# Kernel tuning notes

Hardware: AMD Instinct MI355X
Metric: run time of the kernel (lower is better)

Reference implementation:

```python
import jax, jax.numpy as jnp
import numpy as np
from jax import lax


def conv2d(x, w, padding):
    # x: [B,C,H,W], w: [O,I,kh,kw]; torch Conv2d == cross-correlation, same as lax default
    return lax.conv_general_dilated(x, w, (1, 1), padding,
                                    dimension_numbers=('NCHW', 'OIHW', 'NCHW'))


def setup_inputs() -> dict:
    key = jax.random.key(0)
    ks = jax.random.split(key, 16)
    B, C1, C2, H1, W1, H2, W2, ratio = 8, 256, 512, 64, 64, 32, 32, 8
    Cr = C1 // ratio  # 32
    s = 0.05
    return {
        'x1': jax.random.normal(ks[0], (B, C1, H1, W1), jnp.float32),
        'x2': jax.random.normal(ks[1], (B, C2, H2, W2), jnp.float32),
        'wq': jax.random.normal(ks[2], (Cr, C1, 3, 3), jnp.float32) * s,
        'wk': jax.random.normal(ks[3], (Cr, C2, 3, 3), jnp.float32) * s,
        'wv': jax.random.normal(ks[4], (C1, C2, 3, 3), jnp.float32) * s,
        'wc': jax.random.normal(ks[5], (1, C1, 1, 1), jnp.float32) * s,
        'wch': jax.random.normal(ks[6], (C1, C1, 3, 3), jnp.float32) * s,
        'wt1': jax.random.normal(ks[7], (Cr, C1, 1, 1), jnp.float32) * s,
        'bt1': jax.random.normal(ks[8], (Cr,), jnp.float32) * s,
        'ln_g': jnp.ones((Cr, 1, 1), jnp.float32),
        'ln_b': jnp.zeros((Cr, 1, 1), jnp.float32),
        'wt2': jax.random.normal(ks[9], (C1, Cr, 1, 1), jnp.float32) * s,
        'bt2': jax.random.normal(ks[10], (C1,), jnp.float32) * s,
    }


def reference(x1, x2, wq, wk, wv, wc, wch, wt1, bt1, ln_g, ln_b, wt2, bt2):
    B, C1, H1, W1 = x1.shape
    N1 = H1 * W1
    N2 = x2.shape[2] * x2.shape[3]
    eps = 1e-5

    # spatial cross-attention branch
    q = conv2d(x1, wq, 'SAME').reshape(B, -1, N1)          # [B,Cr,N1]
    k = conv2d(x2, wk, 'SAME').reshape(B, -1, N2)          # [B,Cr,N2]
    v = conv2d(x2, wv, 'SAME').reshape(B, C1, N2)          # [B,C1,N2]
    content = jnp.einsum('bcn,bcm->bnm', k, q)             # [B,N2,N1] (key^T @ query)
    content = jax.nn.softmax(content, axis=1)              # softmax over N2 (dim=1)
    att_con = jnp.einsum('bcn,bnm->bcm', v, content).reshape(B, C1, H1, W1) + x1

    # channel attention branch
    cf = conv2d(x1, wc, 'VALID').reshape(B, 1, N1)         # 1x1 conv -> [B,1,N1]
    cf = jax.nn.softmax(cf.transpose(0, 2, 1), axis=1)     # [B,N1,1], softmax over N1
    chf = conv2d(x1, wch, 'SAME').reshape(B, C1, N1)       # [B,C1,N1]
    pool = jnp.einsum('bcn,bno->bco', chf, cf).reshape(B, C1, 1, 1)

    t = conv2d(pool, wt1, 'VALID') + bt1.reshape(1, -1, 1, 1)  # [B,Cr,1,1]
    mu = jnp.mean(t, axis=(1, 2, 3), keepdims=True)
    var = jnp.mean((t - mu) ** 2, axis=(1, 2, 3), keepdims=True)
    t = (t - mu) * lax.rsqrt(var + eps) * ln_g[None] + ln_b[None]
    t = jax.nn.relu(t)
    channel_weight = conv2d(t, wt2, 'VALID') + bt2.reshape(1, -1, 1, 1)  # [B,C1,1,1]

    return att_con + x1 * channel_weight
```

## Files before the change

kernel.cpp:

```cpp
#include <hip/hip_runtime.h>
#include <stdint.h>

#define LL long long

typedef short short8 __attribute__((ext_vector_type(8)));
typedef float f32x4 __attribute__((ext_vector_type(4)));
typedef unsigned int uint2v __attribute__((ext_vector_type(2)));

__device__ __forceinline__ unsigned short f2bf(float f) {
  unsigned u = __float_as_uint(f);
  unsigned r = (u + 0x7fffu + ((u >> 16) & 1u)) >> 16;
  return (unsigned short)r;
}
__device__ __forceinline__ float bf2f(unsigned short h) {
  return __uint_as_float(((unsigned)h) << 16);
}

#define MFMA16(A, B, C) __builtin_amdgcn_mfma_f32_16x16x32_bf16(A, B, C, 0, 0, 0)

__global__ __launch_bounds__(256) void wtrans2(
    const float* __restrict__ src, unsigned short* __restrict__ dh,
    unsigned short* __restrict__ dl, int OC, int IC)
{
  const int i = blockIdx.x * 256 + threadIdx.x;
  if (i >= OC * IC * 9) return;
  const int off = i % 9;
  const int rest = i / 9;
  const int ic = rest % IC;
  const int oc = rest / IC;
  const float v = src[i];
  const unsigned short h = f2bf(v);
  const LL di = (((LL)off * (IC >> 5) + (ic >> 5)) * OC + oc) * 32 + (ic & 31);
  dh[di] = h;
  if (dl) dl[di] = f2bf(v - bf2f(h));
}

__global__ __launch_bounds__(256) void transp(
    const float* __restrict__ src, unsigned short* __restrict__ dh,
    unsigned short* __restrict__ dl, int C, int N)
{
  __shared__ unsigned short sh[64 * 66];
  __shared__ unsigned short sl[64 * 66];
  const int t = threadIdx.x;
  const int b = blockIdx.z;
  const int n0 = blockIdx.x * 64, c0 = blockIdx.y * 64;
  {
    const int nl = t & 63, cl0 = t >> 6;
#pragma unroll
    for (int i = 0; i < 16; ++i) {
      const int cl = cl0 + 4 * i;
      const float v = src[((LL)b * C + c0 + cl) * N + n0 + nl];
      const unsigned short h = f2bf(v);
      sh[nl * 66 + cl] = h;
      sl[nl * 66 + cl] = f2bf(v - bf2f(h));
    }
  }
  __syncthreads();
  {
    const int cl = t & 63, nr0 = t >> 6;
    const int chunk = (c0 + cl) >> 5;
    const int cin = cl & 31;
#pragma unroll
    for (int j = 0; j < 16; ++j) {
      const int nr = nr0 + 4 * j;
      const LL di = (((LL)b * (C >> 5) + chunk) * N + n0 + nr) * 32 + cin;
      dh[di] = sh[nr * 66 + cl];
      if (dl) dl[di] = sl[nr * 66 + cl];
    }
  }
}

template<int NW>
__global__ __launch_bounds__(NW * 64) void conv_qk_s(
    const unsigned short* __restrict__ xh, const unsigned short* __restrict__ xl,
    const unsigned short* __restrict__ wh, const unsigned short* __restrict__ wl,
    unsigned short* __restrict__ dh, unsigned short* __restrict__ dl,
    int logW, int H)
{
  __shared__ float sred[NW][16][64];
  const int t = threadIdx.x, w = t >> 6, lane = t & 63;
  const int lo4 = lane & 15, hi4 = lane >> 4;
  const int b = blockIdx.z;
  const int W = 1 << logW;
  const int N = H * W;
  const int px0 = blockIdx.x * 32;
  const int row = px0 >> logW;
  const int x0 = px0 & (W - 1);
  const int ch = w;
  const short8 zero8 = {0, 0, 0, 0, 0, 0, 0, 0};

  f32x4 acc[2][2];
#pragma unroll
  for (int p = 0; p < 2; ++p)
#pragma unroll
    for (int ot = 0; ot < 2; ++ot) acc[p][ot] = (f32x4){0.f, 0.f, 0.f, 0.f};

  const LL xbase = ((LL)(b * NW + ch)) * N * 32 + hi4 * 8;
#pragma unroll
  for (int ky = 0; ky < 3; ++ky) {
    const int gy = row + ky - 1;
    const bool oky = (unsigned)gy < (unsigned)H;
    const int gyc = min(max(gy, 0), H - 1);
#pragma unroll
    for (int kx = 0; kx < 3; ++kx) {
      short8 Bh[2], Bl[2];
#pragma unroll
      for (int p = 0; p < 2; ++p) {
        const int gx = x0 + p * 16 + lo4 + kx - 1;
        const bool ok = oky && ((unsigned)gx < (unsigned)W);
        const int gxc = min(max(gx, 0), W - 1);
        const LL xoff = xbase + (LL)(gyc * W + gxc) * 32;
        const short8 bh = *(const short8*)(xh + xoff);
        const short8 bl = *(const short8*)(xl + xoff);
        Bh[p] = ok ? bh : zero8;
        Bl[p] = ok ? bl : zero8;
      }
      const int off = ky * 3 + kx;
      short8 Ah[2], Al[2];
#pragma unroll
      for (int ot = 0; ot < 2; ++ot) {
        const LL wi = ((LL)(off * NW + ch) * 32 + ot * 16 + lo4) * 32 + hi4 * 8;
        Ah[ot] = *(const short8*)(wh + wi);
        Al[ot] = *(const short8*)(wl + wi);
      }
#pragma unroll
      for (int p = 0; p < 2; ++p)
#pragma unroll
        for (int ot = 0; ot < 2; ++ot) {
          acc[p][ot] = MFMA16(Ah[ot], Bh[p], acc[p][ot]);
          acc[p][ot] = MFMA16(Ah[ot], Bl[p], acc[p][ot]);
          acc[p][ot] = MFMA16(Al[ot], Bh[p], acc[p][ot]);
        }
    }
  }
#pragma unroll
  for (int p = 0; p < 2; ++p)
#pragma unroll
    for (int ot = 0; ot < 2; ++ot)
#pragma unroll
      for (int r = 0; r < 4; ++r)
        sred[w][p * 8 + ot * 4 + r][lane] = acc[p][ot][r];
  __syncthreads();
  constexpr int SPW = 16 / NW;
#pragma unroll
  for (int si = 0; si < SPW; ++si) {
    const int slot = w * SPW + si;
    float v = sred[0][slot][lane];
#pragma unroll
    for (int j = 1; j < NW; ++j) v += sred[j][slot][lane];
    const int p = slot >> 3, ot = (slot >> 2) & 1, r = slot & 3;
    const LL di = ((LL)b * N + px0 + p * 16 + lo4) * 32 + ot * 16 + hi4 * 4 + r;
    const unsigned short h = f2bf(v);
    dh[di] = h;
    dl[di] = f2bf(v - bf2f(h));
  }
}

__global__ __launch_bounds__(512) void conv_v_w(
    const unsigned short* __restrict__ xh, const unsigned short* __restrict__ wt,
    unsigned short* __restrict__ out)
{
  __shared__ float sred[4][32][64];
  const int t = threadIdx.x, w = t >> 6, lane = t & 63;
  const int lo4 = lane & 15, hi4 = lane >> 4;
  const int b = blockIdx.z;
  const int h = w & 1, ocg = (w >> 1) & 1, kp = w >> 2;
  const int r0 = blockIdx.x * 4;
  const int ocb = blockIdx.y * 64 + ocg * 32;
  const short8 zero8 = {0, 0, 0, 0, 0, 0, 0, 0};

  f32x4 acc[4][2];
#pragma unroll
  for (int rr = 0; rr < 4; ++rr)
#pragma unroll
    for (int ot = 0; ot < 2; ++ot) acc[rr][ot] = (f32x4){0.f, 0.f, 0.f, 0.f};

  for (int ch = kp * 8; ch < kp * 8 + 8; ++ch) {
    short8 A[3][3][2];
#pragma unroll
    for (int ky = 0; ky < 3; ++ky)
#pragma unroll
      for (int kx = 0; kx < 3; ++kx)
#pragma unroll
        for (int ot = 0; ot < 2; ++ot) {
          const int off = ky * 3 + kx;
          A[ky][kx][ot] = *(const short8*)(
              wt + ((LL)(off * 16 + ch) * 256 + ocb + ot * 16 + lo4) * 32 + hi4 * 8);
        }
    const LL xchb = ((LL)(b * 16 + ch)) * 1024 * 32 + hi4 * 8;
#pragma unroll
    for (int g = 0; g < 6; ++g) {
      const int gy = r0 - 1 + g;
      const bool oky = (unsigned)gy < 32u;
      const int gyc = min(max(gy, 0), 31);
      short8 Bg[3];
#pragma unroll
      for (int kx = 0; kx < 3; ++kx) {
        const int gx = h * 16 + lo4 + kx - 1;
        const bool ok = oky && ((unsigned)gx < 32u);
        const int gxc = min(max(gx, 0), 31);
        const short8 bv = *(const short8*)(xh + xchb + (LL)(gyc * 32 + gxc) * 32);
        Bg[kx] = ok ? bv : zero8;
      }
#pragma unroll
      for (int rr = 0; rr < 4; ++rr) {
        if (rr > g || rr + 2 < g) continue;
        const int ky = g - rr;
#pragma unroll
        for (int kx = 0; kx < 3; ++kx)
#pragma unroll
          for (int ot = 0; ot < 2; ++ot)
            acc[rr][ot] = MFMA16(A[ky][kx][ot], Bg[kx], acc[rr][ot]);
      }
    }
  }
  const int slotbase = h * 2 + ocg;
  if (kp == 1) {
#pragma unroll
    for (int rr = 0; rr < 4; ++rr)
#pragma unroll
      for (int ot = 0; ot < 2; ++ot)
#pragma unroll
        for (int r = 0; r < 4; ++r)
          sred[slotbase][rr * 8 + ot * 4 + r][lane] = acc[rr][ot][r];
  }
  __syncthreads();
  if (kp == 0) {
#pragma unroll
    for (int rr = 0; rr < 4; ++rr)
#pragma unroll
      for (int ot = 0; ot < 2; ++ot)
#pragma unroll
        for (int r = 0; r < 4; ++r) {
          const float v = acc[rr][ot][r] + sred[slotbase][rr * 8 + ot * 4 + r][lane];
          const int row = r0 + rr;
          const int oc = ocb + ot * 16 + hi4 * 4 + r;
          out[(((LL)b * 32 + row) * 256 + oc) * 32 + h * 16 + lo4] = f2bf(v);
        }
  }
}

__global__ __launch_bounds__(256) void cf_dot(
    const float* __restrict__ x1, const float* __restrict__ wc, float* __restrict__ cf)
{
  const int b = blockIdx.y;
  const int n = blockIdx.x * 256 + threadIdx.x;
  const float* xp = x1 + (LL)b * 256 * 4096 + n;
  float a = 0.f;
#pragma unroll 4
  for (int c = 0; c < 256; ++c)
    a = fmaf(xp[(LL)c * 4096], wc[c], a);
  cf[b * 4096 + n] = a;
}

__global__ __launch_bounds__(1024) void cf_softmax(
    const float* __restrict__ cf, float* __restrict__ cfs)
{
  const int b = blockIdx.x, t = threadIdx.x;
  __shared__ float r1[16];
  __shared__ float r2[16];
  float v[4];
#pragma unroll
  for (int j = 0; j < 4; ++j) v[j] = cf[b * 4096 + t + 1024 * j];
  float mx = fmaxf(fmaxf(v[0], v[1]), fmaxf(v[2], v[3]));
#pragma unroll
  for (int k = 1; k <= 32; k <<= 1) mx = fmaxf(mx, __shfl_xor(mx, k));
  const int wv = t >> 6;
  if ((t & 63) == 0) r1[wv] = mx;
  __syncthreads();
  float m2 = r1[0];
#pragma unroll
  for (int i = 1; i < 16; ++i) m2 = fmaxf(m2, r1[i]);
  float e[4]; float s = 0.f;
#pragma unroll
  for (int j = 0; j < 4; ++j) { e[j] = __expf(v[j] - m2); s += e[j]; }
#pragma unroll
  for (int k = 1; k <= 32; k <<= 1) s += __shfl_xor(s, k);
  if ((t & 63) == 0) r2[wv] = s;
  __syncthreads();
  float s2 = 0.f;
#pragma unroll
  for (int i = 0; i < 16; ++i) s2 += r2[i];
  const float inv = 1.f / s2;
#pragma unroll
  for (int j = 0; j < 4; ++j) cfs[b * 4096 + t + 1024 * j] = e[j] * inv;
}

__global__ __launch_bounds__(512) void ykern2(
    const float* __restrict__ x1, const float* __restrict__ cfs,
    float* __restrict__ ykp)
{
  __shared__ __align__(16) float cl2[64][4];
  __shared__ float sredY[256][9];
  const int t = threadIdx.x;
  const int c = t & 255, h = t >> 8;
  const int bx = blockIdx.x, b = blockIdx.y;
  const int base = bx * 2;
  if (t < 256) {
    const int r = t >> 6, cc = t & 63;
    const int grow = base - 1 + r;
    cl2[cc][r] = ((unsigned)grow < 64u) ? cfs[b * 4096 + grow * 64 + cc] : 0.f;
  }
  __syncthreads();
  const int row = base + h;
  float xr[66];
  xr[0] = 0.f; xr[65] = 0.f;
  {
    const float4* xp = (const float4*)(x1 + ((LL)(b * 256 + c)) * 4096 + row * 64);
#pragma unroll
    for (int j = 0; j < 16; ++j) {
      const float4 v = xp[j];
      xr[1 + 4 * j] = v.x; xr[2 + 4 * j] = v.y;
      xr[3 + 4 * j] = v.z; xr[4 + 4 * j] = v.w;
    }
  }
  float a[9];
#pragma unroll
  for (int k = 0; k < 9; ++k) a[k] = 0.f;
  const bool h1 = (h == 1);
#pragma unroll
  for (int c0 = 0; c0 < 64; ++c0) {
    const float4 f4 = *(const float4*)&cl2[c0][0];
    const float f_dy0 = h1 ? f4.w : f4.z;
    const float f_dy1 = h1 ? f4.z : f4.y;
    const float f_dy2 = h1 ? f4.y : f4.x;
#pragma unroll
    for (int dx = 0; dx < 3; ++dx) {
      const float xv = xr[c0 + dx];
      a[0 * 3 + dx] = fmaf(xv, f_dy0, a[0 * 3 + dx]);
      a[1 * 3 + dx] = fmaf(xv, f_dy1, a[1 * 3 + dx]);
      a[2 * 3 + dx] = fmaf(xv, f_dy2, a[2 * 3 + dx]);
    }
  }
  if (h1) {
#pragma unroll
    for (int k = 0; k < 9; ++k) sredY[c][k] = a[k];
  }
  __syncthreads();
  if (!h1) {
    float* op = ykp + ((LL)(b * 32 + bx)) * 2304 + c * 9;
#pragma unroll
    for (int k = 0; k < 9; ++k) op[k] = a[k] + sredY[c][k];
  }
}

__global__ __launch_bounds__(256) void red_t(
    const float* __restrict__ src, float* __restrict__ dst)
{
  const int b = blockIdx.y;
  const int i = blockIdx.x * 256 + threadIdx.x;
  if (i >= 576) return;
  const f32x4* sp = (const f32x4*)(src + (LL)b * 32 * 2304);
  f32x4 a = sp[i];
  for (int p = 1; p < 32; ++p) a += sp[p * 576 + i];
  ((f32x4*)(dst + (LL)b * 2304))[i] = a;
}

__global__ __launch_bounds__(256) void pool_k(
    const float* __restrict__ T, const float* __restrict__ wch,
    float* __restrict__ pool)
{
  __shared__ __align__(16) float Tl[2304];
  const int b = blockIdx.y, ocg = blockIdx.x;
  const int t = threadIdx.x, w = t >> 6, lane = t & 63;
  for (int i = t; i < 2304; i += 256) Tl[i] = T[(LL)b * 2304 + i];
  __syncthreads();
  const float4* tp = (const float4*)Tl;
#pragma unroll
  for (int oi = 0; oi < 2; ++oi) {
    const int oc = ocg * 8 + w * 2 + oi;
    const float4* wp = (const float4*)(wch + (LL)oc * 2304);
    float a = 0.f;
#pragma unroll
    for (int j = 0; j < 9; ++j) {
      const int idx = lane + 64 * j;
      float4 w4 = wp[idx], t4 = tp[idx];
      a = fmaf(w4.x, t4.x, a); a = fmaf(w4.y, t4.y, a);
      a = fmaf(w4.z, t4.z, a); a = fmaf(w4.w, t4.w, a);
    }
#pragma unroll
    for (int k = 1; k <= 32; k <<= 1) a += __shfl_xor(a, k);
    if (lane == 0) pool[b * 256 + oc] = a;
  }
}

__global__ __launch_bounds__(256) void chw_tail(
    const float* __restrict__ pool_g,
    const float* __restrict__ wt1, const float* __restrict__ bt1,
    const float* __restrict__ lng, const float* __restrict__ lnb,
    const float* __restrict__ wt2, const float* __restrict__ bt2,
    float* __restrict__ cwp1)
{
  const int b = blockIdx.x, t = threadIdx.x;
  __shared__ float pool[256];
  __shared__ float tt[32];
  pool[t] = pool_g[b * 256 + t];
  __syncthreads();
  if (t < 64) {
    float tv = 0.f;
    if (t < 32) {
      const float* wp = wt1 + (LL)t * 256;
      for (int c = 0; c < 256; ++c) tv = fmaf(wp[c], pool[c], tv);
      tv += bt1[t];
    }
    float s = tv;
#pragma unroll
    for (int k = 1; k <= 16; k <<= 1) s += __shfl_xor(s, k);
    float mu = s * (1.f / 32.f);
    float d = tv - mu;
    float vs = d * d;
#pragma unroll
    for (int k = 1; k <= 16; k <<= 1) vs += __shfl_xor(vs, k);
    float var = vs * (1.f / 32.f);
    if (t < 32) {
      float nrm = d / sqrtf(var + 1e-5f);
      float y = nrm * lng[t] + lnb[t];
      tt[t] = fmaxf(y, 0.f);
    }
  }
  __syncthreads();
  {
    float s2 = bt2[t];
    const float* wp = wt2 + (LL)t * 32;
#pragma unroll
    for (int i = 0; i < 32; ++i) s2 = fmaf(wp[i], tt[i], s2);
    cwp1[b * 256 + t] = 1.f + s2;
  }
}

__global__ __launch_bounds__(256) void attn_stats(
    const unsigned short* __restrict__ qh_g, const unsigned short* __restrict__ ql_g,
    const unsigned short* __restrict__ kh_g, const unsigned short* __restrict__ kl_g,
    float* __restrict__ mxs, float* __restrict__ invl)
{
  const int t = threadIdx.x, w = t >> 6, lane = t & 63;
  const int lo4 = lane & 15, hi4 = lane >> 4;
  const int b = blockIdx.y, mc = blockIdx.x * 64;
  const float L2E = 1.4426950408889634f;

  short8 qh[4], ql[4];
#pragma unroll
  for (int mt = 0; mt < 4; ++mt) {
    const LL qa = ((LL)(b * 4096 + mc + mt * 16 + lo4)) * 32 + hi4 * 8;
    qh[mt] = *(const short8*)(qh_g + qa);
    ql[mt] = *(const short8*)(ql_g + qa);
  }

  float M[4], L[4];
#pragma unroll
  for (int mt = 0; mt < 4; ++mt) { M[mt] = -1e30f; L[mt] = 0.f; }

  for (int ns = 0; ns < 16; ++ns) {
    const int n = w * 256 + ns * 16 + lo4;
    const LL ka = ((LL)(b * 1024 + n)) * 32 + hi4 * 8;
    const short8 kh = *(const short8*)(kh_g + ka);
    const short8 kl = *(const short8*)(kl_g + ka);
#pragma unroll
    for (int mt = 0; mt < 4; ++mt) {
      f32x4 s = {0.f, 0.f, 0.f, 0.f};
      s = MFMA16(kl, qh[mt], s);
      s = MFMA16(kh, ql[mt], s);
      s = MFMA16(kh, qh[mt], s);
      float lm = fmaxf(fmaxf(s[0], s[1]), fmaxf(s[2], s[3]));
      float nM = fmaxf(M[mt], lm);
      float sc = exp2f((M[mt] - nM) * L2E);
      L[mt] = L[mt] * sc + exp2f((s[0] - nM) * L2E) + exp2f((s[1] - nM) * L2E)
                         + exp2f((s[2] - nM) * L2E) + exp2f((s[3] - nM) * L2E);
      M[mt] = nM;
    }
  }
#pragma unroll
  for (int mask = 16; mask <= 32; mask <<= 1) {
#pragma unroll
    for (int mt = 0; mt < 4; ++mt) {
      float oM = __shfl_xor(M[mt], mask), oL = __shfl_xor(L[mt], mask);
      float nM = fmaxf(M[mt], oM);
      L[mt] = L[mt] * exp2f((M[mt] - nM) * L2E) + oL * exp2f((oM - nM) * L2E);
      M[mt] = nM;
    }
  }
  __shared__ float sM[4][64], sL[4][64];
  if (lane < 16) {
#pragma unroll
    for (int mt = 0; mt < 4; ++mt) {
      sM[w][mt * 16 + lane] = M[mt];
      sL[w][mt * 16 + lane] = L[mt];
    }
  }
  __syncthreads();
  if (t < 64) {
    float Mg = sM[0][t], Lg = sL[0][t];
#pragma unroll
    for (int wv = 1; wv < 4; ++wv) {
      float oM = sM[wv][t], oL = sL[wv][t];
      float nM = fmaxf(Mg, oM);
      Lg = Lg * exp2f((Mg - nM) * L2E) + oL * exp2f((oM - nM) * L2E);
      Mg = nM;
    }
    mxs[b * 4096 + mc + t] = Mg * L2E;
    invl[b * 4096 + mc + t] = 1.f / Lg;
  }
}

__global__ __launch_bounds__(256) void attn_pv(
    const unsigned short* __restrict__ qh_g, const unsigned short* __restrict__ ql_g,
    const unsigned short* __restrict__ kh_g, const unsigned short* __restrict__ kl_g,
    const unsigned short* __restrict__ v16,
    const float* __restrict__ mxs, const float* __restrict__ invl,
    const float* __restrict__ x1, const float* __restrict__ cwp1,
    float* __restrict__ out)
{
  __shared__ __align__(16) unsigned short Pt[2][32][136];
  const int t = threadIdx.x, w = t >> 6, lane = t & 63;
  const int lo4 = lane & 15, hi4 = lane >> 4;
  const int b = blockIdx.y, mb = blockIdx.x * 32;
  const float L2E = 1.4426950408889634f;

  short8 qh[2], ql[2];
  float mxv[2], ilv[2];
#pragma unroll
  for (int mt = 0; mt < 2; ++mt) {
    const int m = mb + mt * 16 + lo4;
    const LL qa = ((LL)(b * 4096 + m)) * 32 + hi4 * 8;
    qh[mt] = *(const short8*)(qh_g + qa);
    ql[mt] = *(const short8*)(ql_g + qa);
    mxv[mt] = mxs[b * 4096 + m];
    ilv[mt] = invl[b * 4096 + m];
  }

  f32x4 acc[4][2];
#pragma unroll
  for (int ct = 0; ct < 4; ++ct)
#pragma unroll
    for (int mt = 0; mt < 2; ++mt) acc[ct][mt] = (f32x4){0.f, 0.f, 0.f, 0.f};

  short8 kh[2], kl[2];
#pragma unroll
  for (int ns = 0; ns < 2; ++ns) {
    const LL ka = ((LL)(b * 1024 + w * 32 + ns * 16 + lo4)) * 32 + hi4 * 8;
    kh[ns] = *(const short8*)(kh_g + ka);
    kl[ns] = *(const short8*)(kl_g + ka);
  }

  int buf = 0;
  for (int nt = 0; nt < 8; ++nt) {
    short8 knh[2], knl[2];
    {
      const int ntn = (nt + 1) & 7;
#pragma unroll
      for (int ns = 0; ns < 2; ++ns) {
        const LL ka = ((LL)(b * 1024 + ntn * 128 + w * 32 + ns * 16 + lo4)) * 32 + hi4 * 8;
        knh[ns] = *(const short8*)(kh_g + ka);
        knl[ns] = *(const short8*)(kl_g + ka);
      }
    }
    f32x4 s[2][2];
#pragma unroll
    for (int ns = 0; ns < 2; ++ns)
#pragma unroll
      for (int mt = 0; mt < 2; ++mt) {
        f32x4 z = {0.f, 0.f, 0.f, 0.f};
        z = MFMA16(kl[ns], qh[mt], z);
        z = MFMA16(kh[ns], ql[mt], z);
        z = MFMA16(kh[ns], qh[mt], z);
        s[ns][mt] = z;
      }
    short8 vpre[2][4];
#pragma unroll
    for (int ks = 0; ks < 2; ++ks)
#pragma unroll
      for (int ct = 0; ct < 4; ++ct)
        vpre[ks][ct] = *(const short8*)(
            v16 + (((LL)b * 32 + nt * 4 + ks) * 256 + w * 64 + ct * 16 + lo4) * 32 + hi4 * 8);
#pragma unroll
    for (int ns = 0; ns < 2; ++ns)
#pragma unroll
      for (int mt = 0; mt < 2; ++mt) {
        const int m_loc = mt * 16 + lo4;
        const int nl = w * 32 + ns * 16 + hi4 * 4;
        float p0 = exp2f(fmaf(s[ns][mt][0], L2E, -mxv[mt])) * ilv[mt];
        float p1 = exp2f(fmaf(s[ns][mt][1], L2E, -mxv[mt])) * ilv[mt];
        float p2 = exp2f(fmaf(s[ns][mt][2], L2E, -mxv[mt])) * ilv[mt];
        float p3 = exp2f(fmaf(s[ns][mt][3], L2E, -mxv[mt])) * ilv[mt];
        uint2v u;
        u[0] = (unsigned)f2bf(p0) | ((unsigned)f2bf(p1) << 16);
        u[1] = (unsigned)f2bf(p2) | ((unsigned)f2bf(p3) << 16);
        *(uint2v*)&Pt[buf][m_loc][nl] = u;
      }
    __syncthreads();
#pragma unroll
    for (int ks = 0; ks < 4; ++ks) {
      short8 pb[2];
#pragma unroll
      for (int mt = 0; mt < 2; ++mt)
        pb[mt] = *(const short8*)&Pt[buf][mt * 16 + lo4][ks * 32 + hi4 * 8];
#pragma unroll
      for (int ct = 0; ct < 4; ++ct) {
        const short8 va = (ks < 2)
            ? vpre[ks][ct]
            : *(const short8*)(
                  v16 + (((LL)b * 32 + nt * 4 + ks) * 256 + w * 64 + ct * 16 + lo4) * 32 + hi4 * 8);
#pragma unroll
        for (int mt = 0; mt < 2; ++mt)
          acc[ct][mt] = MFMA16(va, pb[mt], acc[ct][mt]);
      }
    }
    buf ^= 1;
#pragma unroll
    for (int ns = 0; ns < 2; ++ns) { kh[ns] = knh[ns]; kl[ns] = knl[ns]; }
  }

#pragma unroll
  for (int ct = 0; ct < 4; ++ct)
#pragma unroll
    for (int mt = 0; mt < 2; ++mt) {
      const int m = mb + mt * 16 + lo4;
#pragma unroll
      for (int r = 0; r < 4; ++r) {
        const int c = w * 64 + ct * 16 + hi4 * 4 + r;
        const float cw = cwp1[b * 256 + c];
        const LL off = ((LL)(b * 256 + c)) * 4096 + m;
        out[off] = acc[ct][mt][r] + x1[off] * cw;
      }
    }
}

extern "C" void kernel_launch(void* const* d_in, const int* in_sizes, int n_in,
                              void* d_out, int out_size, void* d_ws, size_t ws_size,
                              hipStream_t stream) {
  const float* x1  = (const float*)d_in[0];
  const float* x2  = (const float*)d_in[1];
  const float* wq  = (const float*)d_in[2];
  const float* wk  = (const float*)d_in[3];
  const float* wv  = (const float*)d_in[4];
  const float* wc  = (const float*)d_in[5];
  const float* wch = (const float*)d_in[6];
  const float* wt1 = (const float*)d_in[7];
  const float* bt1 = (const float*)d_in[8];
  const float* lng = (const float*)d_in[9];
  const float* lnb = (const float*)d_in[10];
  const float* wt2 = (const float*)d_in[11];
  const float* bt2 = (const float*)d_in[12];
  float* outp = (float*)d_out;

  float* ws   = (float*)d_ws;
  float* qtf  = ws;
  float* ktf  = qtf + 1048576;
  float* mxsb = ktf + 262144;
  float* invb = mxsb + 32768;
  float* cfr  = invb + 32768;
  float* cfs  = cfr + 32768;
  float* Tb   = cfs + 32768;
  float* cwb  = Tb + 18432;
  unsigned short* sbase = (unsigned short*)(cwb + 2048);
  unsigned short* v16  = sbase;
  unsigned short* x1th = v16  + 2097152;
  unsigned short* x1tl = x1th + 8388608;
  unsigned short* x2th = x1tl + 8388608;
  unsigned short* x2tl = x2th + 4194304;
  unsigned short* wvt  = x2tl + 4194304;
  unsigned short* wqh  = wvt  + 1179648;
  unsigned short* wql  = wqh  + 73728;
  unsigned short* wkh  = wql  + 73728;
  unsigned short* wkl  = wkh  + 147456;

  unsigned short* qhg = (unsigned short*)qtf;
  unsigned short* qlg = qhg + 1048576;
  unsigned short* khg = (unsigned short*)ktf;
  unsigned short* klg = khg + 262144;

  float* ykp = (float*)x2th;

  wtrans2<<<dim3(4608), 256, 0, stream>>>(wv, wvt, nullptr, 256, 512);
  wtrans2<<<dim3(288),  256, 0, stream>>>(wq, wqh, wql, 32, 256);
  wtrans2<<<dim3(576),  256, 0, stream>>>(wk, wkh, wkl, 32, 512);

  transp<<<dim3(64, 4, 8), 256, 0, stream>>>(x1, x1th, x1tl, 256, 4096);
  transp<<<dim3(16, 8, 8), 256, 0, stream>>>(x2, x2th, x2tl, 512, 1024);

  conv_qk_s<16><<<dim3(32, 1, 8), 1024, 0, stream>>>(
      x2th, x2tl, wkh, wkl, khg, klg, 5, 32);

  conv_v_w<<<dim3(8, 4, 8), 512, 0, stream>>>(x2th, wvt, v16);

  conv_qk_s<8><<<dim3(128, 1, 8), 512, 0, stream>>>(
      x1th, x1tl, wqh, wql, qhg, qlg, 6, 64);

  cf_dot<<<dim3(16, 8), 256, 0, stream>>>(x1, wc, cfr);
  cf_softmax<<<dim3(8), 1024, 0, stream>>>(cfr, cfs);
  ykern2<<<dim3(32, 8), 512, 0, stream>>>(x1, cfs, ykp);
  red_t<<<dim3(3, 8), 256, 0, stream>>>(ykp, Tb);
  pool_k<<<dim3(32, 8), 256, 0, stream>>>(Tb, wch, cfr);
  chw_tail<<<dim3(8), 256, 0, stream>>>(cfr, wt1, bt1, lng, lnb, wt2, bt2, cwb);

  attn_stats<<<dim3(64, 8), 256, 0, stream>>>(qhg, qlg, khg, klg, mxsb, invb);
  attn_pv<<<dim3(128, 8), 256, 0, stream>>>(qhg, qlg, khg, klg, v16, mxsb, invb, x1, cwb, outp);
}
```

Baseline: 375.5 us.

## Double query tile in attn_pv and fold softmax normalizer into exponent bias

```diff
diff --git a/kernel.cpp b/kernel.cpp
--- a/kernel.cpp
+++ b/kernel.cpp
@@ -431,7 +431,7 @@
 __global__ __launch_bounds__(256) void attn_stats(
     const unsigned short* __restrict__ qh_g, const unsigned short* __restrict__ ql_g,
     const unsigned short* __restrict__ kh_g, const unsigned short* __restrict__ kl_g,
-    float* __restrict__ mxs, float* __restrict__ invl)
+    float* __restrict__ subb)
 {
   const int t = threadIdx.x, w = t >> 6, lane = t & 63;
   const int lo4 = lane & 15, hi4 = lane >> 4;
@@ -497,42 +497,40 @@
       Lg = Lg * exp2f((Mg - nM) * L2E) + oL * exp2f((oM - nM) * L2E);
       Mg = nM;
     }
-    mxs[b * 4096 + mc + t] = Mg * L2E;
-    invl[b * 4096 + mc + t] = 1.f / Lg;
-  }
-}
-
-__global__ __launch_bounds__(256) void attn_pv(
+    subb[b * 4096 + mc + t] = -(Mg * L2E + log2f(Lg));
+  }
+}
+
+__global__ __launch_bounds__(256, 2) void attn_pv(
     const unsigned short* __restrict__ qh_g, const unsigned short* __restrict__ ql_g,
     const unsigned short* __restrict__ kh_g, const unsigned short* __restrict__ kl_g,
     const unsigned short* __restrict__ v16,
-    const float* __restrict__ mxs, const float* __restrict__ invl,
+    const float* __restrict__ subb,
     const float* __restrict__ x1, const float* __restrict__ cwp1,
     float* __restrict__ out)
 {
-  __shared__ __align__(16) unsigned short Pt[2][32][136];
+  __shared__ __align__(16) unsigned short Pt[2][64][140];
   const int t = threadIdx.x, w = t >> 6, lane = t & 63;
   const int lo4 = lane & 15, hi4 = lane >> 4;
-  const int b = blockIdx.y, mb = blockIdx.x * 32;
+  const int b = blockIdx.y, mb = blockIdx.x * 64;
   const float L2E = 1.4426950408889634f;
 
-  short8 qh[2], ql[2];
-  float mxv[2], ilv[2];
-#pragma unroll
-  for (int mt = 0; mt < 2; ++mt) {
+  short8 qh[4], ql[4];
+  float sub[4];
+#pragma unroll
+  for (int mt = 0; mt < 4; ++mt) {
     const int m = mb + mt * 16 + lo4;
     const LL qa = ((LL)(b * 4096 + m)) * 32 + hi4 * 8;
     qh[mt] = *(const short8*)(qh_g + qa);
     ql[mt] = *(const short8*)(ql_g + qa);
-    mxv[mt] = mxs[b * 4096 + m];
-    ilv[mt] = invl[b * 4096 + m];
-  }
-
-  f32x4 acc[4][2];
+    sub[mt] = subb[b * 4096 + m];
+  }
+
+  f32x4 acc[4][4];
 #pragma unroll
   for (int ct = 0; ct < 4; ++ct)
 #pragma unroll
-    for (int mt = 0; mt < 2; ++mt) acc[ct][mt] = (f32x4){0.f, 0.f, 0.f, 0.f};
+    for (int mt = 0; mt < 4; ++mt) acc[ct][mt] = (f32x4){0.f, 0.f, 0.f, 0.f};
 
   short8 kh[2], kl[2];
 #pragma unroll
@@ -544,6 +542,13 @@
 
   int buf = 0;
   for (int nt = 0; nt < 8; ++nt) {
+    short8 vpre[2][4];
+#pragma unroll
+    for (int ks = 0; ks < 2; ++ks)
+#pragma unroll
+      for (int ct = 0; ct < 4; ++ct)
+        vpre[ks][ct] = *(const short8*)(
+            v16 + (((LL)b * 32 + nt * 4 + ks) * 256 + w * 64 + ct * 16 + lo4) * 32 + hi4 * 8);
     short8 knh[2], knl[2];
     {
       const int ntn = (nt + 1) & 7;
@@ -554,45 +559,37 @@
         knl[ns] = *(const short8*)(kl_g + ka);
       }
     }
-    f32x4 s[2][2];
-#pragma unroll
-    for (int ns = 0; ns < 2; ++ns)
-#pragma unroll
-      for (int mt = 0; mt < 2; ++mt) {
+#pragma unroll
+    for (int ns = 0; ns < 2; ++ns) {
+      f32x4 s[4];
+#pragma unroll
+      for (int mt = 0; mt < 4; ++mt) {
         f32x4 z = {0.f, 0.f, 0.f, 0.f};
         z = MFMA16(kl[ns], qh[mt], z);
         z = MFMA16(kh[ns], ql[mt], z);
         z = MFMA16(kh[ns], qh[mt], z);
-        s[ns][mt] = z;
-      }
-    short8 vpre[2][4];
-#pragma unroll
-    for (int ks = 0; ks < 2; ++ks)
-#pragma unroll
-      for (int ct = 0; ct < 4; ++ct)
-        vpre[ks][ct] = *(const short8*)(
-            v16 + (((LL)b * 32 + nt * 4 + ks) * 256 + w * 64 + ct * 16 + lo4) * 32 + hi4 * 8);
-#pragma unroll
-    for (int ns = 0; ns < 2; ++ns)
-#pragma unroll
-      for (int mt = 0; mt < 2; ++mt) {
+        s[mt] = z;
+      }
+      const int nl = w * 32 + ns * 16 + hi4 * 4;
+#pragma unroll
+      for (int mt = 0; mt < 4; ++mt) {
         const int m_loc = mt * 16 + lo4;
-        const int nl = w * 32 + ns * 16 + hi4 * 4;
-        float p0 = exp2f(fmaf(s[ns][mt][0], L2E, -mxv[mt])) * ilv[mt];
-        float p1 = exp2f(fmaf(s[ns][mt][1], L2E, -mxv[mt])) * ilv[mt];
-        float p2 = exp2f(fmaf(s[ns][mt][2], L2E, -mxv[mt])) * ilv[mt];
-        float p3 = exp2f(fmaf(s[ns][mt][3], L2E, -mxv[mt])) * ilv[mt];
+        float p0 = exp2f(fmaf(s[mt][0], L2E, sub[mt]));
+        float p1 = exp2f(fmaf(s[mt][1], L2E, sub[mt]));
+        float p2 = exp2f(fmaf(s[mt][2], L2E, sub[mt]));
+        float p3 = exp2f(fmaf(s[mt][3], L2E, sub[mt]));
         uint2v u;
         u[0] = (unsigned)f2bf(p0) | ((unsigned)f2bf(p1) << 16);
         u[1] = (unsigned)f2bf(p2) | ((unsigned)f2bf(p3) << 16);
         *(uint2v*)&Pt[buf][m_loc][nl] = u;
       }
+    }
     __syncthreads();
 #pragma unroll
     for (int ks = 0; ks < 4; ++ks) {
-      short8 pb[2];
-#pragma unroll
-      for (int mt = 0; mt < 2; ++mt)
+      short8 pb[4];
+#pragma unroll
+      for (int mt = 0; mt < 4; ++mt)
         pb[mt] = *(const short8*)&Pt[buf][mt * 16 + lo4][ks * 32 + hi4 * 8];
 #pragma unroll
       for (int ct = 0; ct < 4; ++ct) {
@@ -601,7 +598,7 @@
             : *(const short8*)(
                   v16 + (((LL)b * 32 + nt * 4 + ks) * 256 + w * 64 + ct * 16 + lo4) * 32 + hi4 * 8);
 #pragma unroll
-        for (int mt = 0; mt < 2; ++mt)
+        for (int mt = 0; mt < 4; ++mt)
           acc[ct][mt] = MFMA16(va, pb[mt], acc[ct][mt]);
       }
     }
@@ -613,7 +610,7 @@
 #pragma unroll
   for (int ct = 0; ct < 4; ++ct)
 #pragma unroll
-    for (int mt = 0; mt < 2; ++mt) {
+    for (int mt = 0; mt < 4; ++mt) {
       const int m = mb + mt * 16 + lo4;
 #pragma unroll
       for (int r = 0; r < 4; ++r) {
@@ -693,6 +690,6 @@
   pool_k<<<dim3(32, 8), 256, 0, stream>>>(Tb, wch, cfr);
   chw_tail<<<dim3(8), 256, 0, stream>>>(cfr, wt1, bt1, lng, lnb, wt2, bt2, cwb);
 
-  attn_stats<<<dim3(64, 8), 256, 0, stream>>>(qhg, qlg, khg, klg, mxsb, invb);
-  attn_pv<<<dim3(128, 8), 256, 0, stream>>>(qhg, qlg, khg, klg, v16, mxsb, invb, x1, cwb, outp);
-}
+  attn_stats<<<dim3(64, 8), 256, 0, stream>>>(qhg, qlg, khg, klg, mxsb);
+  attn_pv<<<dim3(64, 8), 256, 0, stream>>>(qhg, qlg, khg, klg, v16, mxsb, x1, cwb, outp);
+}
```

After: 361.5 us. -3.7%, faster.
